# Performance work log

Measured on AMD Instinct MI355X. Metric: run time of the kernel, lower is better.

Reference implementation:

```python
import jax, jax.numpy as jnp
import numpy as np
from jax import lax

B, T, D, H = 4, 4096, 1024, 8
DK, DV = 1024, 2048          # expand_k=1.0, expand_v=2.0
RANK, MAXL, LOOPD = 16, 8, 128  # lora_rank, max_loops, dim*loop_dim_fraction
THRESH = 0.99
EPS = 1e-6
GK_SCALE = 16.0              # GLA forget-gate temperature


def setup_inputs() -> dict:
    key = jax.random.key(0)
    ks = jax.random.split(key, 16)
    r = lambda i, shape, s=0.02: jax.random.normal(ks[i], shape, jnp.float32) * s
    return {
        "h": jax.random.normal(ks[0], (B, T, D), jnp.float32),
        "e": jax.random.normal(ks[1], (B, T, D), jnp.float32),
        "norm_w": jnp.ones((D,), jnp.float32),
        "out_norm_w": jnp.ones((D,), jnp.float32),
        "Wq": r(2, (D, DK)), "Wk": r(3, (D, DK)), "Wv": r(4, (D, DV)),
        "Wgk": r(5, (D, DK)), "Wg": r(6, (D, DV)), "Wo": r(7, (DV, D)),
        "lora_A": r(8, (MAXL, D, RANK)), "lora_B": r(9, (MAXL, RANK, D)),
        "inj_A": 0.9 * jnp.eye(D, dtype=jnp.float32) + r(10, (D, D)),
        "inj_B": r(11, (D, D)),
        "act_w": r(12, (D,)),
        "act_b": jnp.full((), -2.0, jnp.float32),  # gradual halting
        "loop_table": r(13, (MAXL, LOOPD)),
        "n_loops": 4,
    }


def rmsnorm(x, w):
    return x * lax.rsqrt(jnp.mean(x * x, axis=-1, keepdims=True) + EPS) * w


def gla(x, Wq, Wk, Wv, Wgk, Wg, Wo, num_heads):
    """Gated Linear Attention: data-dependent forget gates, linear-time recurrent scan."""
    b, t, d = x.shape
    dk, dv = Wq.shape[1], Wv.shape[1]
    dkh, dvh = dk // num_heads, dv // num_heads
    q = (x @ Wq).reshape(b, t, num_heads, dkh) * (dkh ** -0.5)
    k = (x @ Wk).reshape(b, t, num_heads, dkh)
    v = (x @ Wv).reshape(b, t, num_heads, dvh)
    # forget gate alpha in (0,1): exp(logsigmoid(gk)/16)
    alpha = jnp.exp(jax.nn.log_sigmoid(x @ Wgk) / GK_SCALE).reshape(b, t, num_heads, dkh)

    def step(S, qkva):  # S: (b, H, dkh, dvh)
        qt, kt, vt, at = qkva
        S = at[..., None] * S + kt[..., None] * vt[..., None, :]
        ot = jnp.einsum('bhk,bhkv->bhv', qt, S)
        return S, ot

    S0 = jnp.zeros((b, num_heads, dkh, dvh), x.dtype)
    xs = (jnp.swapaxes(q, 0, 1), jnp.swapaxes(k, 0, 1),
          jnp.swapaxes(v, 0, 1), jnp.swapaxes(alpha, 0, 1))
    _, o = lax.scan(step, S0, xs)                  # o: (t, b, H, dvh)
    o = jnp.swapaxes(o, 0, 1).reshape(b, t, dv)
    o = o * jax.nn.silu(x @ Wg)                    # output gate
    return o @ Wo


def reference(h, e, norm_w, out_norm_w, Wq, Wk, Wv, Wgk, Wg, Wo,
              lora_A, lora_B, inj_A, inj_B, act_w, act_b, loop_table, n_loops):
    b, t_len, d = h.shape
    halted = jnp.zeros((b, t_len), bool)
    cum = jnp.zeros((b, t_len), h.dtype)
    h_out = jnp.zeros_like(h)
    loopd = loop_table.shape[1]
    for t in range(n_loops):  # small fixed depth loop (structurally distinct LoRA/embed per t)
        # loop index embedding on first loopd channels
        h = h.at[..., :loopd].add(loop_table[t])
        h_norm = rmsnorm(h + e, norm_w)
        g = gla(h_norm, Wq, Wk, Wv, Wgk, Wg, Wo, H)   # dropout: eval mode (identity)
        g = g + (g @ lora_A[t]) @ lora_B[t]            # depth LoRA
        h = h @ inj_A.T + e @ inj_B.T + g              # LTI injection: A.h + B.e + gla
        # ACT halting accumulate
        p = jax.nn.sigmoid(h @ act_w + act_b)          # (b, t_len)
        running = ~halted
        p_eff = jnp.where(running, p, jnp.zeros_like(p))
        new_cum = cum + p_eff
        newly = running & (new_cum >= THRESH)
        w = jnp.where(newly, 1.0 - cum, p_eff)         # remainder for newly-halted
        h_out = h_out + w[..., None] * h
        cum = new_cum
        halted = halted | newly
    return rmsnorm(h_out, out_norm_w)
```

## Files before the change

### kernel.cpp

```cpp
#include <hip/hip_runtime.h>

#define BB 4
#define TT 4096
#define DD 1024
#define HH 8
#define DKK 1024
#define DVV 2048
#define MR (BB*TT)
#define DKH 128
#define DVH 256
#define NLOOPS 4
#define LCH 128
#define NCH (TT/LCH)
#define PADW 136
#define NPROJ 7168

#define WS_NEED 662310912ull

__device__ __attribute__((aligned(256))) unsigned char g_ws[WS_NEED];

typedef __bf16 bf16x8 __attribute__((ext_vector_type(8)));
typedef float  f32x4  __attribute__((ext_vector_type(4)));

__device__ __forceinline__ unsigned short f2bfu(float f) {
    unsigned int u = __builtin_bit_cast(unsigned int, f);
    u += 0x7fffu + ((u >> 16) & 1u);
    return (unsigned short)(u >> 16);
}
__device__ __forceinline__ float bfu2f(unsigned short s) {
    unsigned int u = ((unsigned int)s) << 16;
    return __builtin_bit_cast(float, u);
}

__device__ __forceinline__ void gld_lds16(const void* g, void* l) {
    __builtin_amdgcn_global_load_lds(
        (__attribute__((address_space(1))) void*)const_cast<void*>(g),
        (__attribute__((address_space(3))) void*)l, 16, 0, 0);
}

__global__ __launch_bounds__(256) void k_transpose_bf16(
    const float* __restrict__ in, unsigned short* __restrict__ out, int K, int N)
{
    __shared__ float tile[64][65];
    int k0 = blockIdx.y * 64, n0 = blockIdx.x * 64;
    int tx = threadIdx.x & 63, ty = threadIdx.x >> 6;
    #pragma unroll
    for (int r = 0; r < 64; r += 4)
        tile[ty + r][tx] = in[(size_t)(k0 + ty + r) * N + n0 + tx];
    __syncthreads();
    #pragma unroll
    for (int r = 0; r < 64; r += 4)
        out[(size_t)(n0 + ty + r) * K + k0 + tx] = f2bfu(tile[tx][ty + r]);
}

__global__ __launch_bounds__(256) void k_conv_e(
    const float* __restrict__ e, unsigned short* __restrict__ he)
{
    size_t gid = (size_t)blockIdx.x * 256 + threadIdx.x;
    size_t b4 = gid * 4;
    size_t row = b4 >> 10; int col = (int)(b4 & 1023);
    float4 v = *(const float4*)&e[row * 1024 + col];
    *(ushort4*)&he[row * 2048 + 1024 + col] =
        make_ushort4(f2bfu(v.x), f2bfu(v.y), f2bfu(v.z), f2bfu(v.w));
}

__global__ __launch_bounds__(256) void k_conv_injcomb(
    const float* __restrict__ injA, const float* __restrict__ injB,
    unsigned short* __restrict__ WinjT, float* __restrict__ diag)
{
    int idx = blockIdx.x * 256 + threadIdx.x;
    int i = idx >> 10, j = idx & 1023;
    float va = injA[idx], vb = injB[idx];
    unsigned short ua;
    if (i == j) { diag[i] = va; ua = 0; }
    else        { ua = f2bfu(va); }
    WinjT[(size_t)i * 2048 + j] = ua;
    WinjT[(size_t)i * 2048 + 1024 + j] = f2bfu(vb);
}

__global__ __launch_bounds__(256) void k_prep(
    float* __restrict__ h, const float* __restrict__ e,
    const float* __restrict__ norm_w, const float* __restrict__ ltab,
    unsigned short* __restrict__ he, unsigned short* __restrict__ xn_bf)
{
    int row = blockIdx.x, tid = threadIdx.x;
    size_t base = (size_t)row * DD + tid * 4;
    float4 hv = *(float4*)&h[base];
    if (tid < 32) {
        float4 lv = *(const float4*)&ltab[tid * 4];
        hv.x += lv.x; hv.y += lv.y; hv.z += lv.z; hv.w += lv.w;
        *(float4*)&h[base] = hv;
    }
    float4 ev = *(const float4*)&e[base];
    float sx = hv.x + ev.x, sy = hv.y + ev.y, sz = hv.z + ev.z, sw = hv.w + ev.w;
    float partial = sx*sx + sy*sy + sz*sz + sw*sw;
    __shared__ float red[256];
    red[tid] = partial; __syncthreads();
    for (int st = 128; st > 0; st >>= 1) {
        if (tid < st) red[tid] += red[tid + st];
        __syncthreads();
    }
    float rms = rsqrtf(red[0] * (1.0f / DD) + 1e-6f);
    float4 wv = *(const float4*)&norm_w[tid * 4];
    *(ushort4*)&xn_bf[base] = make_ushort4(
        f2bfu(sx * rms * wv.x), f2bfu(sy * rms * wv.y),
        f2bfu(sz * rms * wv.z), f2bfu(sw * rms * wv.w));
    *(ushort4*)&he[(size_t)row * 2048 + tid * 4] =
        make_ushort4(f2bfu(hv.x), f2bfu(hv.y), f2bfu(hv.z), f2bfu(hv.w));
}

template<int KB>
__device__ __forceinline__ void gemm8_core(
    const char* __restrict__ Ab, const char* __restrict__ Bb,
    int bm, int bn, char* sm, f32x4 (&acc)[8][4])
{
    constexpr int NKT = KB / 128;
    const int tid = threadIdx.x;
    const int lane = tid & 63;
    const int wave = tid >> 6;
    const int wm = wave >> 2, wn = wave & 3;
    const int ln15 = lane & 15, q4 = lane >> 4;
    const int xorv = (ln15 & 7) << 4;
    const int xc0 = (q4 * 16) ^ xorv;
    const int xc1 = (64 + q4 * 16) ^ xorv;

    const int L0 = tid * 16;
    const int L1 = 8192 + tid * 16;
    const int lin0 = L0 ^ (((L0 >> 7) & 7) << 4);
    const int lin1 = L1 ^ (((L1 >> 7) & 7) << 4);
    const int sr0 = lin0 >> 7, sc0 = lin0 & 127;
    const int sr1 = lin1 >> 7, sc1 = lin1 & 127;

    bf16x8 av[4][2];
    bf16x8 bv[2][2][2];

    auto STAGE = [&](const char* gb, int row0, int kcol, int region) {
        gld_lds16(gb + (size_t)(row0 + sr0) * KB + (kcol + sc0), sm + region + L0);
        gld_lds16(gb + (size_t)(row0 + sr1) * KB + (kcol + sc1), sm + region + L1);
    };

#define LD_AV(CB, MH) \
    _Pragma("unroll") \
    for (int i2 = 0; i2 < 4; ++i2) { \
        const char* rp = sm + (CB) + ((MH) * 16384) \
                       + ((wm * 64 + i2 * 16 + ln15) * 128); \
        av[i2][0] = *(const bf16x8*)(rp + xc0); \
        av[i2][1] = *(const bf16x8*)(rp + xc1); \
    }
#define LD_BV(CB, NH) \
    _Pragma("unroll") \
    for (int j2 = 0; j2 < 2; ++j2) { \
        const char* rp = sm + (CB) + 32768 + ((NH) * 16384) \
                       + ((wn * 32 + j2 * 16 + ln15) * 128); \
        bv[NH][j2][0] = *(const bf16x8*)(rp + xc0); \
        bv[NH][j2][1] = *(const bf16x8*)(rp + xc1); \
    }
#define MFMA_Q(MH, NH) \
    __builtin_amdgcn_s_setprio(1); \
    _Pragma("unroll") \
    for (int i2 = 0; i2 < 4; ++i2) \
        _Pragma("unroll") \
        for (int j2 = 0; j2 < 2; ++j2) { \
            acc[(MH)*4+i2][(NH)*2+j2] = __builtin_amdgcn_mfma_f32_16x16x32_bf16( \
                av[i2][0], bv[NH][j2][0], acc[(MH)*4+i2][(NH)*2+j2], 0, 0, 0); \
            acc[(MH)*4+i2][(NH)*2+j2] = __builtin_amdgcn_mfma_f32_16x16x32_bf16( \
                av[i2][1], bv[NH][j2][1], acc[(MH)*4+i2][(NH)*2+j2], 0, 0, 0); \
        } \
    __builtin_amdgcn_s_setprio(0);

    STAGE(Ab, bm,       0, 0);
    STAGE(Bb, bn,       0, 32768);
    STAGE(Bb, bn + 128, 0, 49152);
    STAGE(Ab, bm + 128, 0, 16384);

    #pragma unroll 2
    for (int kt = 0; kt < NKT - 1; ++kt) {
        const int cb = (kt & 1) << 16;
        const int sb = cb ^ 65536;
        const int kcol = (kt + 1) * 128;
        STAGE(Ab, bm, kcol, sb);
        asm volatile("s_waitcnt vmcnt(6)" ::: "memory");
        __builtin_amdgcn_s_barrier();
        LD_AV(cb, 0)
        LD_BV(cb, 0)
        MFMA_Q(0, 0)
        STAGE(Bb, bn, kcol, sb + 32768);
        asm volatile("s_waitcnt vmcnt(6)" ::: "memory");
        __builtin_amdgcn_s_barrier();
        LD_BV(cb, 1)
        MFMA_Q(0, 1)
        STAGE(Bb, bn + 128, kcol, sb + 49152);
        asm volatile("s_waitcnt vmcnt(6)" ::: "memory");
        __builtin_amdgcn_s_barrier();
        LD_AV(cb, 1)
        MFMA_Q(1, 1)
        STAGE(Ab, bm + 128, kcol, sb + 16384);
        MFMA_Q(1, 0)
    }
    {
        const int cb = ((NKT - 1) & 1) << 16;
        asm volatile("s_waitcnt vmcnt(4)" ::: "memory");
        __builtin_amdgcn_s_barrier();
        LD_AV(cb, 0)
        LD_BV(cb, 0)
        MFMA_Q(0, 0)
        asm volatile("s_waitcnt vmcnt(2)" ::: "memory");
        __builtin_amdgcn_s_barrier();
        LD_BV(cb, 1)
        MFMA_Q(0, 1)
        asm volatile("s_waitcnt vmcnt(0)" ::: "memory");
        __builtin_amdgcn_s_barrier();
        LD_AV(cb, 1)
        MFMA_Q(1, 1)
        MFMA_Q(1, 0)
    }
#undef LD_AV
#undef LD_BV
#undef MFMA_Q
}

__global__ __launch_bounds__(512, 2) void k_gemm_proj8(
    const unsigned short* __restrict__ A, const unsigned short* __restrict__ Bt,
    unsigned short* __restrict__ qout, unsigned short* __restrict__ kout,
    float* __restrict__ lgout, unsigned short* __restrict__ vout,
    unsigned short* __restrict__ xgout, float qscale)
{
    extern __shared__ char sm[];
    int bid = blockIdx.x;
    int nb = (bid & 7) * 224 + (bid >> 3);
    int bm = (nb / 28) * 256, bn = (nb % 28) * 256;

    f32x4 acc[8][4];
    #pragma unroll
    for (int i = 0; i < 8; ++i)
        #pragma unroll
        for (int j = 0; j < 4; ++j) { f32x4 z = {0,0,0,0}; acc[i][j] = z; }

    gemm8_core<2048>((const char*)A, (const char*)Bt, bm, bn, sm, acc);

    const int tid = threadIdx.x, lane = tid & 63, wave = tid >> 6;
    const int wm = wave >> 2, wn = wave & 3;
    const int ln15 = lane & 15, q4 = lane >> 4;

    if (bn >= 2048 && bn < 3072) {
        int cb = bn - 2048;
        #pragma unroll
        for (int fm = 0; fm < 8; ++fm) {
            int mh = fm >> 2, i2 = fm & 3;
            int rowb = bm + mh * 128 + wm * 64 + i2 * 16 + q4 * 4;
            #pragma unroll
            for (int fn = 0; fn < 4; ++fn) {
                int nh = fn >> 1, j2 = fn & 1;
                int col = cb + nh * 128 + wn * 32 + j2 * 16 + ln15;
                #pragma unroll
                for (int r = 0; r < 4; ++r) {
                    float v = acc[fm][fn][r];
                    v = (fminf(v, 0.f) - log1pf(expf(-fabsf(v)))) * 0.0625f;
                    lgout[(size_t)(rowb + r) * 1024 + col] = v;
                }
            }
        }
    } else {
        unsigned short* obuf; int stride, cb;
        float scale = 1.f;
        if (bn < 1024)      { obuf = qout;  stride = 1024; cb = bn;        scale = qscale; }
        else if (bn < 2048) { obuf = kout;  stride = 1024; cb = bn - 1024; }
        else if (bn < 5120) { obuf = vout;  stride = 2048; cb = bn - 3072; }
        else                { obuf = xgout; stride = 2048; cb = bn - 5120; }
        #pragma unroll
        for (int fm = 0; fm < 8; ++fm) {
            int mh = fm >> 2, i2 = fm & 3;
            int rowb = bm + mh * 128 + wm * 64 + i2 * 16 + q4 * 4;
            #pragma unroll
            for (int fn = 0; fn < 4; ++fn) {
                int nh = fn >> 1, j2 = fn & 1;
                int col = cb + nh * 128 + wn * 32 + j2 * 16 + ln15;
                #pragma unroll
                for (int r = 0; r < 4; ++r)
                    obuf[(size_t)(rowb + r) * stride + col] =
                        f2bfu(acc[fm][fn][r] * scale);
            }
        }
    }
}

template<int HASADD, int HASDIAG, int KB>
__global__ __launch_bounds__(512, 2) void k_gemm8_f32(
    const unsigned short* __restrict__ A, const unsigned short* __restrict__ Bt,
    float* __restrict__ out, const float* __restrict__ addend,
    const float* __restrict__ hsrc, const float* __restrict__ diag, int N)
{
    extern __shared__ char sm[];
    int bid = blockIdx.x;
    int cpx = gridDim.x >> 3;
    int nb = (bid & 7) * cpx + (bid >> 3);
    int nbn = N >> 8;
    int bm = (nb / nbn) * 256, bn = (nb % nbn) * 256;

    f32x4 acc[8][4];
    #pragma unroll
    for (int i = 0; i < 8; ++i)
        #pragma unroll
        for (int j = 0; j < 4; ++j) { f32x4 z = {0,0,0,0}; acc[i][j] = z; }

    gemm8_core<KB>((const char*)A, (const char*)Bt, bm, bn, sm, acc);

    const int tid = threadIdx.x, lane = tid & 63, wave = tid >> 6;
    const int wm = wave >> 2, wn = wave & 3;
    const int ln15 = lane & 15, q4 = lane >> 4;

    #pragma unroll
    for (int fm = 0; fm < 8; ++fm) {
        int mh = fm >> 2, i2 = fm & 3;
        int rowb = bm + mh * 128 + wm * 64 + i2 * 16 + q4 * 4;
        #pragma unroll
        for (int fn = 0; fn < 4; ++fn) {
            int nh = fn >> 1, j2 = fn & 1;
            int col = bn + nh * 128 + wn * 32 + j2 * 16 + ln15;
            float dg = 0.f;
            if (HASDIAG) dg = diag[col];
            #pragma unroll
            for (int r = 0; r < 4; ++r) {
                size_t oi = (size_t)(rowb + r) * N + col;
                float v = acc[fm][fn][r];
                if (HASDIAG) v += hsrc[oi] * dg;
                if (HASADD)  v += addend[oi];
                out[oi] = v;
            }
        }
    }
}

__global__ __launch_bounds__(256) void k_c1(
    const float* __restrict__ lg, unsigned short* __restrict__ q,
    unsigned short* __restrict__ kk, float* __restrict__ dLe)
{
    int chunk = blockIdx.x;
    int bh = blockIdx.y * 2 + (threadIdx.x >> 7);
    int b = bh >> 3, h = bh & 7;
    int i = threadIdx.x & 127;
    size_t r0 = (size_t)b * TT + (size_t)chunk * LCH;
    float c = 0.f, e = 1.f;
    for (int t = 0; t < LCH; ++t) {
        size_t off = (r0 + t) * DKK + h * DKH + i;
        c += lg[off];
        e = __expf(c);
        float ei = __expf(-c);
        q[off] = f2bfu(bfu2f(q[off]) * e);
        kk[off] = f2bfu(bfu2f(kk[off]) * ei);
    }
    dLe[((size_t)chunk * 32 + bh) * DKH + i] = e;
}

__global__ __launch_bounds__(256, 1) void k_c2(
    const unsigned short* __restrict__ q, const unsigned short* __restrict__ kk,
    const unsigned short* __restrict__ v, unsigned short* __restrict__ ob,
    float* __restrict__ U)
{
    extern __shared__ unsigned short smd[];
    unsigned short* lQ  = smd;
    unsigned short* lK  = smd + LCH * PADW;
    unsigned short* lKT = smd + 2 * LCH * PADW;
    unsigned short* lVT = smd + 3 * LCH * PADW;

    int chunk = blockIdx.x, bh = blockIdx.y;
    int b = bh >> 3, h = bh & 7;
    int tid = threadIdx.x, lane = tid & 63, wave = tid >> 6;
    int wm = wave >> 1, wn = wave & 1;
    int quad = lane >> 4, mr = lane & 15;
    size_t r0 = (size_t)b * TT + (size_t)chunk * LCH;

    #pragma unroll
    for (int ps = 0; ps < 8; ++ps) {
        int idx = ps * 256 + tid;
        int row = idx >> 4, c8 = (idx & 15) * 8;
        size_t g = (r0 + row) * DKK + h * DKH + c8;
        *(int4*)&lQ[row * PADW + c8] = *(const int4*)&q[g];
        union { int4 w; unsigned short u[8]; } tmp;
        tmp.w = *(const int4*)&kk[g];
        *(int4*)&lK[row * PADW + c8] = tmp.w;
        #pragma unroll
        for (int u2 = 0; u2 < 8; ++u2)
            lKT[(c8 + u2) * PADW + row] = tmp.u[u2];
    }
    __syncthreads();

    f32x4 pa[4][4];
    #pragma unroll
    for (int i = 0; i < 4; ++i)
        #pragma unroll
        for (int j = 0; j < 4; ++j) { f32x4 z = {0,0,0,0}; pa[i][j] = z; }
    for (int k0 = 0; k0 < DKH; k0 += 32) {
        bf16x8 av[4], bv[4];
        #pragma unroll
        for (int t2 = 0; t2 < 4; ++t2) {
            av[t2] = *(const bf16x8*)&lQ[(wm * 64 + t2 * 16 + mr) * PADW + k0 + quad * 8];
            bv[t2] = *(const bf16x8*)&lK[(wn * 64 + t2 * 16 + mr) * PADW + k0 + quad * 8];
        }
        #pragma unroll
        for (int tm = 0; tm < 4; ++tm)
            #pragma unroll
            for (int tn = 0; tn < 4; ++tn)
                pa[tm][tn] = __builtin_amdgcn_mfma_f32_16x16x32_bf16(
                    av[tm], bv[tn], pa[tm][tn], 0, 0, 0);
    }
    __syncthreads();

    #pragma unroll
    for (int tm = 0; tm < 4; ++tm)
        #pragma unroll
        for (int tn = 0; tn < 4; ++tn)
            #pragma unroll
            for (int r = 0; r < 4; ++r) {
                int trow = wm * 64 + tm * 16 + quad * 4 + r;
                int scol = wn * 64 + tn * 16 + mr;
                float pv = (trow >= scol) ? pa[tm][tn][r] : 0.f;
                lQ[trow * PADW + scol] = f2bfu(pv);
            }
    #pragma unroll
    for (int ps = 0; ps < 8; ++ps) {
        int idx = ps * 256 + tid;
        int s = idx >> 4, j8 = (idx & 15) * 8;
        size_t g = (r0 + s) * DVV + h * DVH + j8;
        union { int4 w; unsigned short u[8]; } tmp;
        tmp.w = *(const int4*)&v[g];
        #pragma unroll
        for (int u2 = 0; u2 < 8; ++u2)
            lVT[(j8 + u2) * PADW + s] = tmp.u[u2];
    }
    __syncthreads();

    #pragma unroll 1
    for (int panel = 0; panel < 2; ++panel) {
        f32x4 oa[4][4], ua[4][4];
        #pragma unroll
        for (int i = 0; i < 4; ++i)
            #pragma unroll
            for (int j = 0; j < 4; ++j) { f32x4 z = {0,0,0,0}; oa[i][j] = z; ua[i][j] = z; }
        for (int k0 = 0; k0 < LCH; k0 += 32) {
            bf16x8 pv[4], kt[4], vb[4];
            #pragma unroll
            for (int t2 = 0; t2 < 4; ++t2) {
                pv[t2] = *(const bf16x8*)&lQ [(wm * 64 + t2 * 16 + mr) * PADW + k0 + quad * 8];
                kt[t2] = *(const bf16x8*)&lKT[(wm * 64 + t2 * 16 + mr) * PADW + k0 + quad * 8];
                vb[t2] = *(const bf16x8*)&lVT[(wn * 64 + t2 * 16 + mr) * PADW + k0 + quad * 8];
            }
            #pragma unroll
            for (int tm = 0; tm < 4; ++tm)
                #pragma unroll
                for (int tn = 0; tn < 4; ++tn) {
                    oa[tm][tn] = __builtin_amdgcn_mfma_f32_16x16x32_bf16(
                        pv[tm], vb[tn], oa[tm][tn], 0, 0, 0);
                    ua[tm][tn] = __builtin_amdgcn_mfma_f32_16x16x32_bf16(
                        kt[tm], vb[tn], ua[tm][tn], 0, 0, 0);
                }
        }
        #pragma unroll
        for (int tm = 0; tm < 4; ++tm)
            #pragma unroll
            for (int tn = 0; tn < 4; ++tn)
                #pragma unroll
                for (int r = 0; r < 4; ++r) {
                    int m_ = wm * 64 + tm * 16 + quad * 4 + r;
                    int j_ = panel * 128 + wn * 64 + tn * 16 + mr;
                    ob[(r0 + m_) * DVV + h * DVH + j_] = f2bfu(oa[tm][tn][r]);
                    U[(((size_t)chunk * 32 + bh) * DKH + m_) * DVH + j_] = ua[tm][tn][r];
                }
        __syncthreads();
        if (panel == 0) {
            #pragma unroll
            for (int ps = 0; ps < 8; ++ps) {
                int idx = ps * 256 + tid;
                int s = idx >> 4, j8 = (idx & 15) * 8;
                size_t g = (r0 + s) * DVV + h * DVH + 128 + j8;
                union { int4 w; unsigned short u[8]; } tmp;
                tmp.w = *(const int4*)&v[g];
                #pragma unroll
                for (int u2 = 0; u2 < 8; ++u2)
                    lVT[(j8 + u2) * PADW + s] = tmp.u[u2];
            }
            __syncthreads();
        }
    }
}

__global__ __launch_bounds__(256) void k_c3(
    float* __restrict__ U, const float* __restrict__ dLe)
{
    int gid = blockIdx.x * 256 + threadIdx.x;
    int bh = gid >> 13;
    int rem = gid & 8191;
    int i = rem >> 6, j4 = rem & 63;
    float4 S = make_float4(0.f, 0.f, 0.f, 0.f);
    for (int c = 0; c < NCH; ++c) {
        size_t off = (((size_t)c * 32 + bh) * DKH + i) * DVH + j4 * 4;
        float4 u = *(float4*)&U[off];
        *(float4*)&U[off] = S;
        float d = dLe[((size_t)c * 32 + bh) * DKH + i];
        S.x = d * (S.x + u.x); S.y = d * (S.y + u.y);
        S.z = d * (S.z + u.z); S.w = d * (S.w + u.w);
    }
}

__global__ __launch_bounds__(256, 1) void k_c4(
    const unsigned short* __restrict__ q, const float* __restrict__ S,
    unsigned short* __restrict__ ob, const unsigned short* __restrict__ xg)
{
    extern __shared__ unsigned short smd[];
    unsigned short* lQ  = smd;
    unsigned short* lST = smd + LCH * PADW;

    int chunk = blockIdx.x, bh = blockIdx.y;
    int b = bh >> 3, h = bh & 7;
    int tid = threadIdx.x, lane = tid & 63, wave = tid >> 6;
    int wm = wave >> 1, wn = wave & 1;
    int quad = lane >> 4, mr = lane & 15;
    size_t r0 = (size_t)b * TT + (size_t)chunk * LCH;

    #pragma unroll
    for (int ps = 0; ps < 8; ++ps) {
        int idx = ps * 256 + tid;
        int row = idx >> 4, c8 = (idx & 15) * 8;
        size_t g = (r0 + row) * DKK + h * DKH + c8;
        *(int4*)&lQ[row * PADW + c8] = *(const int4*)&q[g];
    }

    #pragma unroll 1
    for (int panel = 0; panel < 2; ++panel) {
        __syncthreads();
        #pragma unroll
        for (int ps = 0; ps < 16; ++ps) {
            int idx = ps * 256 + tid;
            int i = idx >> 5, j4 = idx & 31;
            float4 sv = *(const float4*)&S[(((size_t)chunk * 32 + bh) * DKH + i) * DVH
                                           + panel * 128 + j4 * 4];
            lST[(j4 * 4 + 0) * PADW + i] = f2bfu(sv.x);
            lST[(j4 * 4 + 1) * PADW + i] = f2bfu(sv.y);
            lST[(j4 * 4 + 2) * PADW + i] = f2bfu(sv.z);
            lST[(j4 * 4 + 3) * PADW + i] = f2bfu(sv.w);
        }
        __syncthreads();

        f32x4 oa[4][4];
        #pragma unroll
        for (int i = 0; i < 4; ++i)
            #pragma unroll
            for (int j = 0; j < 4; ++j) { f32x4 z = {0,0,0,0}; oa[i][j] = z; }
        for (int k0 = 0; k0 < DKH; k0 += 32) {
            bf16x8 av[4], bv[4];
            #pragma unroll
            for (int t2 = 0; t2 < 4; ++t2) {
                av[t2] = *(const bf16x8*)&lQ [(wm * 64 + t2 * 16 + mr) * PADW + k0 + quad * 8];
                bv[t2] = *(const bf16x8*)&lST[(wn * 64 + t2 * 16 + mr) * PADW + k0 + quad * 8];
            }
            #pragma unroll
            for (int tm = 0; tm < 4; ++tm)
                #pragma unroll
                for (int tn = 0; tn < 4; ++tn)
                    oa[tm][tn] = __builtin_amdgcn_mfma_f32_16x16x32_bf16(
                        av[tm], bv[tn], oa[tm][tn], 0, 0, 0);
        }
        #pragma unroll
        for (int tm = 0; tm < 4; ++tm)
            #pragma unroll
            for (int tn = 0; tn < 4; ++tn)
                #pragma unroll
                for (int r = 0; r < 4; ++r) {
                    int t_ = wm * 64 + tm * 16 + quad * 4 + r;
                    int j_ = panel * 128 + wn * 64 + tn * 16 + mr;
                    size_t oi = (r0 + t_) * DVV + h * DVH + j_;
                    float ov = bfu2f(ob[oi]) + oa[tm][tn][r];
                    float xf = bfu2f(xg[oi]);
                    ob[oi] = f2bfu(ov * xf / (1.f + expf(-xf)));
                }
    }
}

__global__ __launch_bounds__(256) void k_lora1(
    const float* __restrict__ G, const float* __restrict__ A, float* __restrict__ tmp)
{
    int row = blockIdx.x * 4 + (threadIdx.x >> 6);
    int lane = threadIdx.x & 63;
    float acc[16];
    #pragma unroll
    for (int r = 0; r < 16; ++r) acc[r] = 0.f;
    const float* grow = G + (size_t)row * DD;
    for (int k2 = lane; k2 < DD; k2 += 64) {
        float g = grow[k2];
        const float4* ar = (const float4*)(A + k2 * 16);
        float4 a0 = ar[0], a1 = ar[1], a2 = ar[2], a3 = ar[3];
        acc[0] = fmaf(g, a0.x, acc[0]);  acc[1] = fmaf(g, a0.y, acc[1]);
        acc[2] = fmaf(g, a0.z, acc[2]);  acc[3] = fmaf(g, a0.w, acc[3]);
        acc[4] = fmaf(g, a1.x, acc[4]);  acc[5] = fmaf(g, a1.y, acc[5]);
        acc[6] = fmaf(g, a1.z, acc[6]);  acc[7] = fmaf(g, a1.w, acc[7]);
        acc[8] = fmaf(g, a2.x, acc[8]);  acc[9] = fmaf(g, a2.y, acc[9]);
        acc[10] = fmaf(g, a2.z, acc[10]); acc[11] = fmaf(g, a2.w, acc[11]);
        acc[12] = fmaf(g, a3.x, acc[12]); acc[13] = fmaf(g, a3.y, acc[13]);
        acc[14] = fmaf(g, a3.z, acc[14]); acc[15] = fmaf(g, a3.w, acc[15]);
    }
    #pragma unroll
    for (int off = 32; off >= 1; off >>= 1)
        #pragma unroll
        for (int r = 0; r < 16; ++r) acc[r] += __shfl_xor(acc[r], off);
    if (lane == 0) {
        #pragma unroll
        for (int r = 0; r < 16; ++r) tmp[(size_t)row * 16 + r] = acc[r];
    }
}

__global__ __launch_bounds__(256) void k_lora2(
    float* __restrict__ G, const float* __restrict__ tmp, const float* __restrict__ Bm)
{
    int row = blockIdx.x, tid = threadIdx.x;
    __shared__ float t16[16];
    if (tid < 16) t16[tid] = tmp[(size_t)row * 16 + tid];
    __syncthreads();
    size_t base = (size_t)row * DD + tid * 4;
    float4 acc = *(float4*)&G[base];
    #pragma unroll
    for (int r = 0; r < 16; ++r) {
        float tv = t16[r];
        float4 bv = *(const float4*)&Bm[r * DD + tid * 4];
        acc.x = fmaf(tv, bv.x, acc.x); acc.y = fmaf(tv, bv.y, acc.y);
        acc.z = fmaf(tv, bv.z, acc.z); acc.w = fmaf(tv, bv.w, acc.w);
    }
    *(float4*)&G[base] = acc;
}

__global__ __launch_bounds__(256) void k_act(
    const float* __restrict__ h, const float* __restrict__ act_w,
    const float* __restrict__ act_b, float* __restrict__ out,
    float* __restrict__ cum, int* __restrict__ halted)
{
    int row = blockIdx.x, tid = threadIdx.x;
    size_t base = (size_t)row * DD + tid * 4;
    float4 hv = *(const float4*)&h[base];
    float4 wv = *(const float4*)&act_w[tid * 4];
    float partial = hv.x*wv.x + hv.y*wv.y + hv.z*wv.z + hv.w*wv.w;
    __shared__ float red[256];
    __shared__ float s_cm;
    __shared__ int s_hl;
    if (tid == 0) { s_cm = cum[row]; s_hl = halted[row]; }
    red[tid] = partial; __syncthreads();
    for (int st = 128; st > 0; st >>= 1) {
        if (tid < st) red[tid] += red[tid + st];
        __syncthreads();
    }
    float p = 1.f / (1.f + expf(-(red[0] + act_b[0])));
    float cm = s_cm;
    int hl = s_hl;
    float p_eff = hl ? 0.f : p;
    float ncum = cm + p_eff;
    int newly = (!hl) && (ncum >= 0.99f);
    float w = newly ? (1.f - cm) : p_eff;
    float4 ho = *(float4*)&out[base];
    ho.x += w * hv.x; ho.y += w * hv.y; ho.z += w * hv.z; ho.w += w * hv.w;
    *(float4*)&out[base] = ho;
    if (tid == 0) { cum[row] = ncum; halted[row] = hl | newly; }
}

__global__ __launch_bounds__(256) void k_final(
    float* __restrict__ io, const float* __restrict__ w)
{
    int row = blockIdx.x, tid = threadIdx.x;
    size_t base = (size_t)row * DD + tid * 4;
    float4 hv = *(const float4*)&io[base];
    float partial = hv.x*hv.x + hv.y*hv.y + hv.z*hv.z + hv.w*hv.w;
    __shared__ float red[256];
    red[tid] = partial; __syncthreads();
    for (int st = 128; st > 0; st >>= 1) {
        if (tid < st) red[tid] += red[tid + st];
        __syncthreads();
    }
    float rms = rsqrtf(red[0] * (1.0f / DD) + 1e-6f);
    float4 wv = *(const float4*)&w[tid * 4];
    float4 o = make_float4(hv.x*rms*wv.x, hv.y*rms*wv.y, hv.z*rms*wv.z, hv.w*rms*wv.w);
    *(float4*)&io[base] = o;
}

extern "C" void kernel_launch(void* const* d_in, const int* in_sizes, int n_in,
                              void* d_out, int out_size, void* d_ws, size_t ws_size,
                              hipStream_t stream)
{
    const float* in_h       = (const float*)d_in[0];
    const float* in_e       = (const float*)d_in[1];
    const float* norm_w     = (const float*)d_in[2];
    const float* out_norm_w = (const float*)d_in[3];
    const float* Wq   = (const float*)d_in[4];
    const float* Wk   = (const float*)d_in[5];
    const float* Wv   = (const float*)d_in[6];
    const float* Wgk  = (const float*)d_in[7];
    const float* Wg   = (const float*)d_in[8];
    const float* Wo   = (const float*)d_in[9];
    const float* lora_A = (const float*)d_in[10];
    const float* lora_B = (const float*)d_in[11];
    const float* inj_A  = (const float*)d_in[12];
    const float* inj_B  = (const float*)d_in[13];
    const float* act_w  = (const float*)d_in[14];
    const float* act_b  = (const float*)d_in[15];
    const float* loop_table = (const float*)d_in[16];

    char* p;
    if (ws_size >= WS_NEED) {
        p = (char*)d_ws;
    } else {
        void* sym = nullptr;
        hipGetSymbolAddress(&sym, HIP_SYMBOL(g_ws));
        p = (char*)sym;
    }

    float* h      = (float*)p;            p += (size_t)MR * DD * 4;
    unsigned short* he_bf = (unsigned short*)p; p += (size_t)MR * 2048 * 2;
    unsigned short* xn_bf = (unsigned short*)p; p += (size_t)MR * DD * 2;
    unsigned short* q_bf  = (unsigned short*)p; p += (size_t)MR * DKK * 2;
    unsigned short* k_bf  = (unsigned short*)p; p += (size_t)MR * DKK * 2;
    unsigned short* v_bf  = (unsigned short*)p; p += (size_t)MR * DVV * 2;
    unsigned short* xg_bf = (unsigned short*)p; p += (size_t)MR * DVV * 2;
    float* lgbuf  = (float*)p;            p += (size_t)MR * DKK * 4;
    unsigned short* ob0   = (unsigned short*)p; p += (size_t)MR * DVV * 2;
    float* U      = (float*)p;            p += (size_t)NCH * 32 * DKH * DVH * 4;
    float* dLe    = (float*)p;            p += (size_t)NCH * 32 * DKH * 4;
    unsigned short* WprojT = (unsigned short*)p; p += (size_t)NPROJ * DKK * 2;
    unsigned short* WoT    = (unsigned short*)p; p += (size_t)DD * DVV * 2;
    unsigned short* WinjT  = (unsigned short*)p; p += (size_t)DD * 2048 * 2;
    float* diagA = (float*)p;             p += DD * 4;
    float* tmp16 = (float*)p;             p += (size_t)MR * 16 * 4;
    float* cum   = (float*)p;             p += MR * 4;
    int*   halted = (int*)p;              p += MR * 4;
    float* g2 = lgbuf;
    float* h_out = (float*)d_out;

    hipMemcpyAsync(h, in_h, (size_t)MR * DD * 4, hipMemcpyDeviceToDevice, stream);
    hipMemsetAsync(h_out, 0, (size_t)MR * DD * 4, stream);
    hipMemsetAsync(cum, 0, MR * 4, stream);
    hipMemsetAsync(halted, 0, MR * 4, stream);

    k_transpose_bf16<<<dim3(16, 16), 256, 0, stream>>>(Wq,  WprojT,              DD, DKK);
    k_transpose_bf16<<<dim3(16, 16), 256, 0, stream>>>(Wk,  WprojT + 1024*1024,  DD, DKK);
    k_transpose_bf16<<<dim3(16, 16), 256, 0, stream>>>(Wgk, WprojT + 2048*1024,  DD, DKK);
    k_transpose_bf16<<<dim3(32, 16), 256, 0, stream>>>(Wv,  WprojT + 3072*1024,  DD, DVV);
    k_transpose_bf16<<<dim3(32, 16), 256, 0, stream>>>(Wg,  WprojT + (size_t)5120*1024, DD, DVV);
    k_transpose_bf16<<<dim3(16, 32), 256, 0, stream>>>(Wo,  WoT, DVV, DD);
    k_conv_injcomb<<<4096, 256, 0, stream>>>(inj_A, inj_B, WinjT, diagA);
    k_conv_e<<<MR * DD / 1024, 256, 0, stream>>>(in_e, he_bf);

    const float qscale = 0.08838834764831845f;

    for (int t = 0; t < NLOOPS; ++t) {
        k_prep<<<MR, 256, 0, stream>>>(h, in_e, norm_w, loop_table + t * 128, he_bf, xn_bf);

        k_gemm_proj8<<<1792, 512, 131072, stream>>>(
            xn_bf, WprojT, q_bf, k_bf, lgbuf, v_bf, xg_bf, qscale);

        k_c1<<<dim3(NCH, 16), 256, 0, stream>>>(lgbuf, q_bf, k_bf, dLe);
        k_c2<<<dim3(NCH, 32), 256, 4 * LCH * PADW * 2, stream>>>(
            q_bf, k_bf, v_bf, ob0, U);
        k_c3<<<1024, 256, 0, stream>>>(U, dLe);
        k_c4<<<dim3(NCH, 32), 256, 2 * LCH * PADW * 2, stream>>>(q_bf, U, ob0, xg_bf);

        k_gemm8_f32<0, 0, 4096><<<256, 512, 131072, stream>>>(
            ob0, WoT, g2, nullptr, nullptr, nullptr, DD);

        k_lora1<<<MR / 4, 256, 0, stream>>>(g2, lora_A + (size_t)t * DD * 16, tmp16);
        k_lora2<<<MR, 256, 0, stream>>>(g2, tmp16, lora_B + (size_t)t * 16 * DD);

        k_gemm8_f32<1, 1, 4096><<<256, 512, 131072, stream>>>(
            he_bf, WinjT, h, g2, h, diagA, DD);

        k_act<<<MR, 256, 0, stream>>>(h, act_w, act_b, h_out, cum, halted);
    }

    k_final<<<MR, 256, 0, stream>>>(h_out, out_norm_w);
}
```

Before: 4.177 ms.

## Fuse LoRA kernels and ACT with next prep, stage projection stores via LDS

Several changes at once. k_lora1 and k_lora2 are merged into one per-row kernel that reduces the rank-16 projection across waves in shared memory. k_act for iterations 0-2 is fused with the next iteration's k_prep, so each iteration reads and writes h once fewer. The projection GEMM epilogue now stages bf16 tiles in LDS and writes coalesced 16-byte rows. The GEMM main loop also drops one barrier per k-step by loading both B halves up front. These cut launches and scattered 2-byte stores, at the cost of a tighter wait schedule and extra LDS pressure.

New measurement: 4.301 ms. 3.0% more time.

```diff
diff --git a/kernel.cpp b/kernel.cpp
--- a/kernel.cpp
+++ b/kernel.cpp
@@ -179,15 +179,13 @@
         const int sb = cb ^ 65536;
         const int kcol = (kt + 1) * 128;
         STAGE(Ab, bm, kcol, sb);
-        asm volatile("s_waitcnt vmcnt(6)" ::: "memory");
+        asm volatile("s_waitcnt vmcnt(4)" ::: "memory");
         __builtin_amdgcn_s_barrier();
         LD_AV(cb, 0)
         LD_BV(cb, 0)
+        LD_BV(cb, 1)
         MFMA_Q(0, 0)
         STAGE(Bb, bn, kcol, sb + 32768);
-        asm volatile("s_waitcnt vmcnt(6)" ::: "memory");
-        __builtin_amdgcn_s_barrier();
-        LD_BV(cb, 1)
         MFMA_Q(0, 1)
         STAGE(Bb, bn + 128, kcol, sb + 49152);
         asm volatile("s_waitcnt vmcnt(6)" ::: "memory");
@@ -199,14 +197,12 @@
     }
     {
         const int cb = ((NKT - 1) & 1) << 16;
-        asm volatile("s_waitcnt vmcnt(4)" ::: "memory");
+        asm volatile("s_waitcnt vmcnt(2)" ::: "memory");
         __builtin_amdgcn_s_barrier();
         LD_AV(cb, 0)
         LD_BV(cb, 0)
+        LD_BV(cb, 1)
         MFMA_Q(0, 0)
-        asm volatile("s_waitcnt vmcnt(2)" ::: "memory");
-        __builtin_amdgcn_s_barrier();
-        LD_BV(cb, 1)
         MFMA_Q(0, 1)
         asm volatile("s_waitcnt vmcnt(0)" ::: "memory");
         __builtin_amdgcn_s_barrier();
@@ -261,24 +257,36 @@
             }
         }
     } else {
-        unsigned short* obuf; int stride, cb;
+        unsigned short* obuf; int stride, cbcol;
         float scale = 1.f;
-        if (bn < 1024)      { obuf = qout;  stride = 1024; cb = bn;        scale = qscale; }
-        else if (bn < 2048) { obuf = kout;  stride = 1024; cb = bn - 1024; }
-        else if (bn < 5120) { obuf = vout;  stride = 2048; cb = bn - 3072; }
-        else                { obuf = xgout; stride = 2048; cb = bn - 5120; }
-        #pragma unroll
-        for (int fm = 0; fm < 8; ++fm) {
-            int mh = fm >> 2, i2 = fm & 3;
-            int rowb = bm + mh * 128 + wm * 64 + i2 * 16 + q4 * 4;
-            #pragma unroll
-            for (int fn = 0; fn < 4; ++fn) {
-                int nh = fn >> 1, j2 = fn & 1;
-                int col = cb + nh * 128 + wn * 32 + j2 * 16 + ln15;
+        if (bn < 1024)      { obuf = qout;  stride = 1024; cbcol = bn;        scale = qscale; }
+        else if (bn < 2048) { obuf = kout;  stride = 1024; cbcol = bn - 1024; }
+        else if (bn < 5120) { obuf = vout;  stride = 2048; cbcol = bn - 3072; }
+        else                { obuf = xgout; stride = 2048; cbcol = bn - 5120; }
+        unsigned short* c16 = (unsigned short*)sm;
+        #pragma unroll
+        for (int half = 0; half < 2; ++half) {
+            if (half) __syncthreads();
+            #pragma unroll
+            for (int i2 = 0; i2 < 4; ++i2) {
+                int lrow0 = wm * 64 + i2 * 16 + q4 * 4;
                 #pragma unroll
-                for (int r = 0; r < 4; ++r)
-                    obuf[(size_t)(rowb + r) * stride + col] =
-                        f2bfu(acc[fm][fn][r] * scale);
+                for (int fn = 0; fn < 4; ++fn) {
+                    int nh = fn >> 1, j2 = fn & 1;
+                    int lcol = nh * 128 + wn * 32 + j2 * 16 + ln15;
+                    #pragma unroll
+                    for (int r = 0; r < 4; ++r)
+                        c16[(lrow0 + r) * 264 + lcol] =
+                            f2bfu(acc[half * 4 + i2][fn][r] * scale);
+                }
+            }
+            __syncthreads();
+            #pragma unroll
+            for (int ps = 0; ps < 8; ++ps) {
+                int idx = ps * 512 + tid;
+                int rl = idx >> 5, c8 = (idx & 31) * 8;
+                int4 w = *(int4*)&c16[rl * 264 + c8];
+                *(int4*)&obuf[(size_t)(bm + half * 128 + rl) * stride + cbcol + c8] = w;
             }
         }
     }
@@ -576,27 +584,32 @@
     }
 }
 
-__global__ __launch_bounds__(256) void k_lora1(
-    const float* __restrict__ G, const float* __restrict__ A, float* __restrict__ tmp)
-{
-    int row = blockIdx.x * 4 + (threadIdx.x >> 6);
-    int lane = threadIdx.x & 63;
+__global__ __launch_bounds__(256) void k_lora12(
+    float* __restrict__ G, const float* __restrict__ A, const float* __restrict__ Bm)
+{
+    int row = blockIdx.x, tid = threadIdx.x;
+    int lane = tid & 63, wave = tid >> 6;
+    __shared__ float wred[4][16];
+    size_t base = (size_t)row * DD + tid * 4;
+    float4 g4 = *(float4*)&G[base];
+    float ga[4] = { g4.x, g4.y, g4.z, g4.w };
     float acc[16];
     #pragma unroll
     for (int r = 0; r < 16; ++r) acc[r] = 0.f;
-    const float* grow = G + (size_t)row * DD;
-    for (int k2 = lane; k2 < DD; k2 += 64) {
-        float g = grow[k2];
-        const float4* ar = (const float4*)(A + k2 * 16);
-        float4 a0 = ar[0], a1 = ar[1], a2 = ar[2], a3 = ar[3];
-        acc[0] = fmaf(g, a0.x, acc[0]);  acc[1] = fmaf(g, a0.y, acc[1]);
-        acc[2] = fmaf(g, a0.z, acc[2]);  acc[3] = fmaf(g, a0.w, acc[3]);
-        acc[4] = fmaf(g, a1.x, acc[4]);  acc[5] = fmaf(g, a1.y, acc[5]);
-        acc[6] = fmaf(g, a1.z, acc[6]);  acc[7] = fmaf(g, a1.w, acc[7]);
-        acc[8] = fmaf(g, a2.x, acc[8]);  acc[9] = fmaf(g, a2.y, acc[9]);
-        acc[10] = fmaf(g, a2.z, acc[10]); acc[11] = fmaf(g, a2.w, acc[11]);
-        acc[12] = fmaf(g, a3.x, acc[12]); acc[13] = fmaf(g, a3.y, acc[13]);
-        acc[14] = fmaf(g, a3.z, acc[14]); acc[15] = fmaf(g, a3.w, acc[15]);
+    const float* a0 = A + (size_t)(tid * 4) * 16;
+    #pragma unroll
+    for (int kk = 0; kk < 4; ++kk) {
+        float g = ga[kk];
+        const float4* ar = (const float4*)(a0 + kk * 16);
+        float4 v0 = ar[0], v1 = ar[1], v2 = ar[2], v3 = ar[3];
+        acc[0]  = fmaf(g, v0.x, acc[0]);  acc[1]  = fmaf(g, v0.y, acc[1]);
+        acc[2]  = fmaf(g, v0.z, acc[2]);  acc[3]  = fmaf(g, v0.w, acc[3]);
+        acc[4]  = fmaf(g, v1.x, acc[4]);  acc[5]  = fmaf(g, v1.y, acc[5]);
+        acc[6]  = fmaf(g, v1.z, acc[6]);  acc[7]  = fmaf(g, v1.w, acc[7]);
+        acc[8]  = fmaf(g, v2.x, acc[8]);  acc[9]  = fmaf(g, v2.y, acc[9]);
+        acc[10] = fmaf(g, v2.z, acc[10]); acc[11] = fmaf(g, v2.w, acc[11]);
+        acc[12] = fmaf(g, v3.x, acc[12]); acc[13] = fmaf(g, v3.y, acc[13]);
+        acc[14] = fmaf(g, v3.z, acc[14]); acc[15] = fmaf(g, v3.w, acc[15]);
     }
     #pragma unroll
     for (int off = 32; off >= 1; off >>= 1)
@@ -604,27 +617,17 @@
         for (int r = 0; r < 16; ++r) acc[r] += __shfl_xor(acc[r], off);
     if (lane == 0) {
         #pragma unroll
-        for (int r = 0; r < 16; ++r) tmp[(size_t)row * 16 + r] = acc[r];
-    }
-}
-
-__global__ __launch_bounds__(256) void k_lora2(
-    float* __restrict__ G, const float* __restrict__ tmp, const float* __restrict__ Bm)
-{
-    int row = blockIdx.x, tid = threadIdx.x;
-    __shared__ float t16[16];
-    if (tid < 16) t16[tid] = tmp[(size_t)row * 16 + tid];
+        for (int r = 0; r < 16; ++r) wred[wave][r] = acc[r];
+    }
     __syncthreads();
-    size_t base = (size_t)row * DD + tid * 4;
-    float4 acc = *(float4*)&G[base];
     #pragma unroll
     for (int r = 0; r < 16; ++r) {
-        float tv = t16[r];
+        float tv = wred[0][r] + wred[1][r] + wred[2][r] + wred[3][r];
         float4 bv = *(const float4*)&Bm[r * DD + tid * 4];
-        acc.x = fmaf(tv, bv.x, acc.x); acc.y = fmaf(tv, bv.y, acc.y);
-        acc.z = fmaf(tv, bv.z, acc.z); acc.w = fmaf(tv, bv.w, acc.w);
-    }
-    *(float4*)&G[base] = acc;
+        g4.x = fmaf(tv, bv.x, g4.x); g4.y = fmaf(tv, bv.y, g4.y);
+        g4.z = fmaf(tv, bv.z, g4.z); g4.w = fmaf(tv, bv.w, g4.w);
+    }
+    *(float4*)&G[base] = g4;
 }
 
 __global__ __launch_bounds__(256) void k_act(
@@ -657,6 +660,63 @@
     ho.x += w * hv.x; ho.y += w * hv.y; ho.z += w * hv.z; ho.w += w * hv.w;
     *(float4*)&out[base] = ho;
     if (tid == 0) { cum[row] = ncum; halted[row] = hl | newly; }
+}
+
+__global__ __launch_bounds__(256) void k_actprep(
+    float* __restrict__ h, const float* __restrict__ e,
+    const float* __restrict__ act_w, const float* __restrict__ act_b,
+    float* __restrict__ out, float* __restrict__ cum, int* __restrict__ halted,
+    const float* __restrict__ norm_w, const float* __restrict__ ltab,
+    unsigned short* __restrict__ he, unsigned short* __restrict__ xn_bf)
+{
+    int row = blockIdx.x, tid = threadIdx.x;
+    size_t base = (size_t)row * DD + tid * 4;
+    float4 hv = *(float4*)&h[base];
+    __shared__ float red[256];
+    __shared__ float s_cm;
+    __shared__ int s_hl;
+    {
+        float4 wv = *(const float4*)&act_w[tid * 4];
+        float partial = hv.x*wv.x + hv.y*wv.y + hv.z*wv.z + hv.w*wv.w;
+        if (tid == 0) { s_cm = cum[row]; s_hl = halted[row]; }
+        red[tid] = partial; __syncthreads();
+        for (int st = 128; st > 0; st >>= 1) {
+            if (tid < st) red[tid] += red[tid + st];
+            __syncthreads();
+        }
+        float p = 1.f / (1.f + expf(-(red[0] + act_b[0])));
+        float cm = s_cm;
+        int hl = s_hl;
+        float p_eff = hl ? 0.f : p;
+        float ncum = cm + p_eff;
+        int newly = (!hl) && (ncum >= 0.99f);
+        float w = newly ? (1.f - cm) : p_eff;
+        float4 ho = *(float4*)&out[base];
+        ho.x += w * hv.x; ho.y += w * hv.y; ho.z += w * hv.z; ho.w += w * hv.w;
+        *(float4*)&out[base] = ho;
+        if (tid == 0) { cum[row] = ncum; halted[row] = hl | newly; }
+    }
+    __syncthreads();
+    if (tid < 32) {
+        float4 lv = *(const float4*)&ltab[tid * 4];
+        hv.x += lv.x; hv.y += lv.y; hv.z += lv.z; hv.w += lv.w;
+        *(float4*)&h[base] = hv;
+    }
+    float4 ev = *(const float4*)&e[base];
+    float sx = hv.x + ev.x, sy = hv.y + ev.y, sz = hv.z + ev.z, sw = hv.w + ev.w;
+    float partial = sx*sx + sy*sy + sz*sz + sw*sw;
+    red[tid] = partial; __syncthreads();
+    for (int st = 128; st > 0; st >>= 1) {
+        if (tid < st) red[tid] += red[tid + st];
+        __syncthreads();
+    }
+    float rms = rsqrtf(red[0] * (1.0f / DD) + 1e-6f);
+    float4 wv = *(const float4*)&norm_w[tid * 4];
+    *(ushort4*)&xn_bf[base] = make_ushort4(
+        f2bfu(sx * rms * wv.x), f2bfu(sy * rms * wv.y),
+        f2bfu(sz * rms * wv.z), f2bfu(sw * rms * wv.w));
+    *(ushort4*)&he[(size_t)row * 2048 + tid * 4] =
+        make_ushort4(f2bfu(hv.x), f2bfu(hv.y), f2bfu(hv.z), f2bfu(hv.w));
 }
 
 __global__ __launch_bounds__(256) void k_final(
@@ -729,6 +789,7 @@
     int*   halted = (int*)p;              p += MR * 4;
     float* g2 = lgbuf;
     float* h_out = (float*)d_out;
+    (void)tmp16;
 
     hipMemcpyAsync(h, in_h, (size_t)MR * DD * 4, hipMemcpyDeviceToDevice, stream);
     hipMemsetAsync(h_out, 0, (size_t)MR * DD * 4, stream);
@@ -746,9 +807,9 @@
 
     const float qscale = 0.08838834764831845f;
 
+    k_prep<<<MR, 256, 0, stream>>>(h, in_e, norm_w, loop_table, he_bf, xn_bf);
+
     for (int t = 0; t < NLOOPS; ++t) {
-        k_prep<<<MR, 256, 0, stream>>>(h, in_e, norm_w, loop_table + t * 128, he_bf, xn_bf);
-
         k_gemm_proj8<<<1792, 512, 131072, stream>>>(
             xn_bf, WprojT, q_bf, k_bf, lgbuf, v_bf, xg_bf, qscale);
 
@@ -761,13 +822,19 @@
         k_gemm8_f32<0, 0, 4096><<<256, 512, 131072, stream>>>(
             ob0, WoT, g2, nullptr, nullptr, nullptr, DD);
 
-        k_lora1<<<MR / 4, 256, 0, stream>>>(g2, lora_A + (size_t)t * DD * 16, tmp16);
-        k_lora2<<<MR, 256, 0, stream>>>(g2, tmp16, lora_B + (size_t)t * 16 * DD);
+        k_lora12<<<MR, 256, 0, stream>>>(
+            g2, lora_A + (size_t)t * DD * 16, lora_B + (size_t)t * 16 * DD);
 
         k_gemm8_f32<1, 1, 4096><<<256, 512, 131072, stream>>>(
             he_bf, WinjT, h, g2, h, diagA, DD);
 
-        k_act<<<MR, 256, 0, stream>>>(h, act_w, act_b, h_out, cum, halted);
+        if (t < NLOOPS - 1) {
+            k_actprep<<<MR, 256, 0, stream>>>(
+                h, in_e, act_w, act_b, h_out, cum, halted,
+                norm_w, loop_table + (t + 1) * 128, he_bf, xn_bf);
+        } else {
+            k_act<<<MR, 256, 0, stream>>>(h, act_w, act_b, h_out, cum, halted);
+        }
     }
 
     k_final<<<MR, 256, 0, stream>>>(h_out, out_norm_w);
```
